# Kernel optimization log

Measured on AMD Instinct MI355X. Metric: run time of the kernel, lower is better.

## Reference

```python
import jax, jax.numpy as jnp
import numpy as np

N, E, F, H, C, K = 50000, 1600000, 128, 64, 40, 4


def setup_inputs() -> dict:
    key = jax.random.key(0)
    ks = jax.random.split(key, 4)
    x = jax.random.normal(ks[0], (N, F), dtype=jnp.float32)
    edge_index = jax.random.randint(ks[1], (2, E), 0, N, dtype=jnp.int32)
    edge_weight = jnp.ones((E,), dtype=jnp.float32)
    # lin of ChebConv: Linear(K*in, out); kaiming for layer1, xavier-ish for layer2
    W1 = jax.random.normal(ks[2], (K * F, H), dtype=jnp.float32) * (2.0 / (K * F)) ** 0.5
    b1 = jnp.zeros((H,), jnp.float32)
    W2 = jax.random.normal(ks[3], (K * H, C), dtype=jnp.float32) * (2.0 / (K * H + C)) ** 0.5
    b2 = jnp.zeros((C,), jnp.float32)
    return {"x": x, "edge_index": edge_index, "edge_weight": edge_weight,
            "W1": W1, "b1": b1, "W2": W2, "b2": b2}


def _cheb_norm(edge_index, edge_weight, num_nodes):
    """Edge weights of L_hat = 2*L/lambda_max - I with sym norm, lambda_max=2.
    L = I - D^{-1/2} A D^{-1/2}; so L_hat off-diag = -d_i^{-1/2} w d_j^{-1/2},
    diag = (1 if deg>0 else 0) - 1."""
    src, dst = edge_index[0], edge_index[1]
    deg = jax.ops.segment_sum(edge_weight, src, num_segments=num_nodes)
    dis = jnp.where(deg > 0, jax.lax.rsqrt(jnp.maximum(deg, 1e-12)), 0.0)
    w_norm = -dis[src] * edge_weight * dis[dst]   # [E] off-diagonal of L_hat
    diag = jnp.where(deg > 0, 0.0, -1.0)          # [N] diagonal of L_hat
    return src, dst, w_norm, diag


def _cheb_conv(x, src, dst, w_norm, diag, W, b, num_nodes):
    def prop(h):  # L_hat @ h via gather-multiply-scatter
        msg = w_norm[:, None] * h[src]                                  # [E, F]
        return diag[:, None] * h + jax.ops.segment_sum(msg, dst, num_segments=num_nodes)

    Tx_prev2 = x
    Tx_prev1 = prop(x)
    Txs = [Tx_prev2, Tx_prev1]
    for _ in range(2, K):
        Tx = 2.0 * prop(Tx_prev1) - Tx_prev2
        Txs.append(Tx)
        Tx_prev2, Tx_prev1 = Tx_prev1, Tx
    Z = jnp.concatenate(Txs, axis=1)              # [N, K*F]
    return Z @ W + b


def reference(x, edge_index, edge_weight, W1, b1, W2, b2):
    num_nodes = x.shape[0]
    src, dst, w_norm, diag = _cheb_norm(edge_index, edge_weight, num_nodes)
    # dropout layers are identity at inference
    h = _cheb_conv(x, src, dst, w_norm, diag, W1, b1, num_nodes)
    h = jax.nn.relu(h)
    out = _cheb_conv(h, src, dst, w_norm, diag, W2, b2, num_nodes)
    return out
```

## Files before the change

kernel.cpp:

```cpp
#include <hip/hip_runtime.h>

#define NN 50000
#define EE 1600000
#define FF 128
#define HH 64
#define CC 40

#define NCH 64
#define CHE (EE / NCH)
#define NSL 4
#define SLN (NN / NSL)

#define PA 250
#define EPP (EE / PA)
#define SB 250
#define SLNB 200
#define BCAP 64

static __device__ __forceinline__ float bf2f(unsigned short u) {
    union { unsigned int i; float f; } c; c.i = ((unsigned int)u) << 16; return c.f;
}
static __device__ __forceinline__ unsigned short f2bf(float x) {
    union { float f; unsigned int i; } c; c.f = x;
    unsigned int r = c.i + 0x7FFFu + ((c.i >> 16) & 1u);
    return (unsigned short)(r >> 16);
}

__global__ __launch_bounds__(1024) void deg_hist_kernel(
    const int* __restrict__ src, const float* __restrict__ w,
    float* __restrict__ pdeg) {
    __shared__ float ldeg[SLN];
    int s = blockIdx.x % NSL;
    int c = blockIdx.x / NSL;
    int base = s * SLN;
    for (int i = threadIdx.x; i < SLN; i += 1024) ldeg[i] = 0.f;
    __syncthreads();
    int e0 = c * CHE;
    for (int e = e0 + threadIdx.x; e < e0 + CHE; e += 1024) {
        int se = src[e];
        unsigned us = (unsigned)(se - base);
        if (us < SLN) atomicAdd(&ldeg[us], w[e]);
    }
    __syncthreads();
    for (int i = threadIdx.x; i < SLN; i += 1024)
        pdeg[(size_t)c * NN + base + i] = ldeg[i];
}

__global__ void reduce_kernel(const float* __restrict__ pdeg,
                              float* __restrict__ dis, float* __restrict__ diag) {
    int n = blockIdx.x * blockDim.x + threadIdx.x;
    if (n >= NN) return;
    float dsum = 0.f;
    for (int c = 0; c < NCH; ++c) dsum += pdeg[(size_t)c * NN + n];
    dis[n]  = (dsum > 0.f) ? rsqrtf(fmaxf(dsum, 1e-12f)) : 0.f;
    diag[n] = (dsum > 0.f) ? 0.f : -1.f;
}

__global__ __launch_bounds__(256) void bucketA_kernel(
    const int* __restrict__ src, const int* __restrict__ dst,
    const float* __restrict__ w, const float* __restrict__ dis,
    uint2* __restrict__ buckets, int* __restrict__ counts) {
    __shared__ int lcnt[SB];
    int p = blockIdx.x;
    for (int i = threadIdx.x; i < SB; i += 256) lcnt[i] = 0;
    __syncthreads();
    int e0 = p * EPP;
    for (int e = e0 + threadIdx.x; e < e0 + EPP; e += 256) {
        int de = dst[e], se = src[e];
        int sl = de / SLNB;
        int dl = de - sl * SLNB;
        float wn = -dis[se] * w[e] * dis[de];
        unsigned lo = (unsigned)se | ((unsigned)f2bf(wn) << 16);
        int idx = atomicAdd(&lcnt[sl], 1);
        buckets[((size_t)p * SB + sl) * BCAP + idx] = make_uint2(lo, (unsigned)dl);
    }
    __syncthreads();
    for (int i = threadIdx.x; i < SB; i += 256) counts[p * SB + i] = lcnt[i];
}

__global__ void scanS_kernel(const int* __restrict__ counts, int* __restrict__ sbase) {
    __shared__ int sh[256];
    int t = threadIdx.x;
    int total = 0;
    if (t < SB)
        for (int p = 0; p < PA; ++p) total += counts[p * SB + t];
    sh[t] = total;
    __syncthreads();
    for (int off = 1; off < 256; off <<= 1) {
        int x = (t >= off) ? sh[t - off] : 0;
        __syncthreads();
        sh[t] += x;
        __syncthreads();
    }
    if (t < SB) sbase[t] = sh[t] - total;
    if (t == SB - 1) sbase[SB] = sh[t];
}

__global__ __launch_bounds__(256) void bucketB_kernel(
    const uint2* __restrict__ buckets, const int* __restrict__ counts,
    const int* __restrict__ sbase,
    int* __restrict__ row_start, unsigned int* __restrict__ csr) {
    __shared__ int lhist[SLNB];
    __shared__ int sh[256];
    int s = blockIdx.x;
    int t = threadIdx.x;
    int lane = t & 63, wave = t >> 6;
    for (int i = t; i < SLNB; i += 256) lhist[i] = 0;
    __syncthreads();
    for (int p = wave; p < PA; p += 4) {
        int c = counts[p * SB + s];
        const uint2* b = buckets + ((size_t)p * SB + s) * BCAP;
        for (int i = lane; i < c; i += 64)
            atomicAdd(&lhist[b[i].y], 1);
    }
    __syncthreads();
    int v = (t < SLNB) ? lhist[t] : 0;
    sh[t] = v;
    __syncthreads();
    for (int off = 1; off < 256; off <<= 1) {
        int x = (t >= off) ? sh[t - off] : 0;
        __syncthreads();
        sh[t] += x;
        __syncthreads();
    }
    int base = sbase[s];
    if (t < SLNB) {
        int excl = sh[t] - v;
        row_start[s * SLNB + t] = base + excl;
        lhist[t] = base + excl;
    }
    if (s == SB - 1 && t == 0) row_start[NN] = sbase[SB];
    __syncthreads();
    for (int p = wave; p < PA; p += 4) {
        int c = counts[p * SB + s];
        const uint2* b = buckets + ((size_t)p * SB + s) * BCAP;
        for (int i = lane; i < c; i += 64) {
            uint2 en = b[i];
            int pos = atomicAdd(&lhist[en.y], 1);
            csr[pos] = en.x;
        }
    }
}

template <int FACT, typename OUT_T>
__global__ __launch_bounds__(256) void prop2_kernel(
    const unsigned short* __restrict__ a, int aStride, float alphaL,
    const float* __restrict__ p1, float beta1,
    const float* __restrict__ p2, float beta2, int pStride,
    const float* __restrict__ bias, int doRelu, int FOUT, int outStride,
    const float* __restrict__ diag, const int* __restrict__ rs,
    const unsigned int* __restrict__ csr, OUT_T* __restrict__ out) {
    int lane = threadIdx.x & 63;
    int wave = threadIdx.x >> 6;
    int n = blockIdx.x * 4 + wave;
    int f = lane;
    float acc = 0.f;
    if (f < FACT) {
        acc = diag[n] * bf2f(a[(size_t)n * aStride + f]);
        int j0 = rs[n], j1 = rs[n + 1];
        int j = j0;
        for (; j + 8 <= j1; j += 8) {
            unsigned cw[8];
            #pragma unroll
            for (int u = 0; u < 8; ++u) cw[u] = csr[j + u];
            float v[8];
            #pragma unroll
            for (int u = 0; u < 8; ++u)
                v[u] = bf2f(a[(size_t)(cw[u] & 0xFFFFu) * aStride + f]);
            #pragma unroll
            for (int u = 0; u < 8; ++u)
                acc = fmaf(bf2f((unsigned short)(cw[u] >> 16)), v[u], acc);
        }
        for (; j < j1; ++j) {
            unsigned cw = csr[j];
            acc = fmaf(bf2f((unsigned short)(cw >> 16)),
                       bf2f(a[(size_t)(cw & 0xFFFFu) * aStride + f]), acc);
        }
    }
    if (f < FOUT) {
        float r = alphaL * acc + beta1 * p1[(size_t)n * pStride + f];
        if (beta2 != 0.f) r = fmaf(beta2, p2[(size_t)n * pStride + f], r);
        if (bias) r += bias[f];
        if (doRelu) r = fmaxf(r, 0.f);
        OUT_T o;
        if constexpr (sizeof(OUT_T) == 2) o = f2bf(r); else o = r;
        out[(size_t)n * outStride + f] = o;
    }
}

__global__ __launch_bounds__(256) void gemm1_kernel(
    const float* __restrict__ x, const float* __restrict__ W,
    float* __restrict__ Yf, unsigned short* __restrict__ y3b) {
    __shared__ float As[64][36];
    __shared__ float Bs[32][64];
    int t = threadIdx.x;
    int m0 = blockIdx.x * 64;
    int ct = blockIdx.y;
    int tr = t / 16, tc = t % 16;
    int kq = t % 8,  ms = t / 8;
    int jb = t % 16, fb = t / 16;
    float acc[4][4] = {};
    for (int kb = 0; kb < 4; ++kb) {
        __syncthreads();
        #pragma unroll
        for (int p = 0; p < 2; ++p) {
            int m = ms + 32 * p;
            int row = m0 + m;
            float4 vv = make_float4(0.f, 0.f, 0.f, 0.f);
            if (row < NN) vv = *(const float4*)(x + (size_t)row * FF + kb * 32 + kq * 4);
            *(float4*)&As[m][kq * 4] = vv;
        }
        const float* Wb = W + ((size_t)ct * 128 + kb * 32) * HH;
        #pragma unroll
        for (int p = 0; p < 2; ++p) {
            int fi = fb + 16 * p;
            float4 vv = *(const float4*)(Wb + fi * HH + jb * 4);
            *(float4*)&Bs[fi][jb * 4] = vv;
        }
        __syncthreads();
        #pragma unroll 8
        for (int k = 0; k < 32; ++k) {
            float a0 = As[tr * 4 + 0][k], a1 = As[tr * 4 + 1][k];
            float a2 = As[tr * 4 + 2][k], a3 = As[tr * 4 + 3][k];
            float4 b = *(float4*)&Bs[k][tc * 4];
            acc[0][0] = fmaf(a0, b.x, acc[0][0]); acc[0][1] = fmaf(a0, b.y, acc[0][1]);
            acc[0][2] = fmaf(a0, b.z, acc[0][2]); acc[0][3] = fmaf(a0, b.w, acc[0][3]);
            acc[1][0] = fmaf(a1, b.x, acc[1][0]); acc[1][1] = fmaf(a1, b.y, acc[1][1]);
            acc[1][2] = fmaf(a1, b.z, acc[1][2]); acc[1][3] = fmaf(a1, b.w, acc[1][3]);
            acc[2][0] = fmaf(a2, b.x, acc[2][0]); acc[2][1] = fmaf(a2, b.y, acc[2][1]);
            acc[2][2] = fmaf(a2, b.z, acc[2][2]); acc[2][3] = fmaf(a2, b.w, acc[2][3]);
            acc[3][0] = fmaf(a3, b.x, acc[3][0]); acc[3][1] = fmaf(a3, b.y, acc[3][1]);
            acc[3][2] = fmaf(a3, b.z, acc[3][2]); acc[3][3] = fmaf(a3, b.w, acc[3][3]);
        }
    }
    #pragma unroll
    for (int r = 0; r < 4; ++r) {
        int n = m0 + tr * 4 + r;
        if (n < NN) {
            *(float4*)(Yf + (size_t)n * 256 + ct * 64 + tc * 4) =
                make_float4(acc[r][0], acc[r][1], acc[r][2], acc[r][3]);
            if (ct == 3) {
                ushort4 u4;
                u4.x = f2bf(acc[r][0]); u4.y = f2bf(acc[r][1]);
                u4.z = f2bf(acc[r][2]); u4.w = f2bf(acc[r][3]);
                *(ushort4*)(y3b + (size_t)n * 64 + tc * 4) = u4;
            }
        }
    }
}

__global__ __launch_bounds__(256) void gemm2_kernel(
    const float* __restrict__ h, const float* __restrict__ W,
    float* __restrict__ Y2f, unsigned short* __restrict__ y3b2) {
    __shared__ float As[128][36];
    __shared__ float Bs[32][40];
    int t = threadIdx.x;
    int m0 = blockIdx.x * 128;
    int kt = blockIdx.y;
    int tr = t / 8, tc = t % 8;
    int kq = t % 8, ms = t / 8;
    float acc[4][5] = {};
    for (int kb = 0; kb < 2; ++kb) {
        __syncthreads();
        #pragma unroll
        for (int p = 0; p < 4; ++p) {
            int m = ms + 32 * p;
            int row = m0 + m;
            float4 vv = make_float4(0.f, 0.f, 0.f, 0.f);
            if (row < NN) vv = *(const float4*)(h + (size_t)row * HH + kb * 32 + kq * 4);
            *(float4*)&As[m][kq * 4] = vv;
        }
        const float* Wb = W + ((size_t)kt * 64 + kb * 32) * CC;
        for (int i = t; i < 32 * CC; i += 256) ((float*)Bs)[i] = Wb[i];
        __syncthreads();
        #pragma unroll 4
        for (int k = 0; k < 32; ++k) {
            float a0 = As[tr * 4 + 0][k], a1 = As[tr * 4 + 1][k];
            float a2 = As[tr * 4 + 2][k], a3 = As[tr * 4 + 3][k];
            #pragma unroll
            for (int c = 0; c < 5; ++c) {
                float b = Bs[k][tc * 5 + c];
                acc[0][c] = fmaf(a0, b, acc[0][c]);
                acc[1][c] = fmaf(a1, b, acc[1][c]);
                acc[2][c] = fmaf(a2, b, acc[2][c]);
                acc[3][c] = fmaf(a3, b, acc[3][c]);
            }
        }
    }
    #pragma unroll
    for (int r = 0; r < 4; ++r) {
        int n = m0 + tr * 4 + r;
        if (n < NN) {
            float* orow = Y2f + (size_t)n * 256 + kt * 64;
            #pragma unroll
            for (int c = 0; c < 5; ++c) orow[tc * 5 + c] = acc[r][c];
            if (tc < 6) {
                #pragma unroll
                for (int c = 0; c < 4; ++c) orow[40 + tc * 4 + c] = 0.f;
            }
            if (kt == 3) {
                unsigned short* brow = y3b2 + (size_t)n * 64;
                #pragma unroll
                for (int c = 0; c < 5; ++c) brow[tc * 5 + c] = f2bf(acc[r][c]);
                if (tc < 6) {
                    #pragma unroll
                    for (int c = 0; c < 4; ++c) brow[40 + tc * 4 + c] = 0;
                }
            }
        }
    }
}

extern "C" void kernel_launch(void* const* d_in, const int* in_sizes, int n_in,
                              void* d_out, int out_size, void* d_ws, size_t ws_size,
                              hipStream_t stream) {
    const float* x    = (const float*)d_in[0];
    const int*   eidx = (const int*)d_in[1];
    const float* ew   = (const float*)d_in[2];
    const float* W1   = (const float*)d_in[3];
    const float* b1   = (const float*)d_in[4];
    const float* W2   = (const float*)d_in[5];
    const float* b2   = (const float*)d_in[6];
    float* out = (float*)d_out;

    const int* src = eidx;
    const int* dst = eidx + EE;

    float* p = (float*)d_ws;
    unsigned int* csr = (unsigned int*)p;  p += (size_t)EE;
    float* dis  = p;                  p += ((NN + 63) / 64) * 64;
    float* diag = p;                  p += ((NN + 63) / 64) * 64;
    float* Yf   = p;                  p += (size_t)NN * 256;
    unsigned short* y3b = (unsigned short*)p;  p += (size_t)NN * 32;
    unsigned short* u   = (unsigned short*)p;  p += (size_t)NN * 32;
    unsigned short* v   = (unsigned short*)p;  p += (size_t)NN * 32;
    float* h    = p;                  p += (size_t)NN * 64;
    int* row_start = (int*)p;
    int* counts    = row_start + NN + 1;
    int* sbase     = counts + PA * SB;

    float* pdeg    = Yf;
    uint2* buckets = (uint2*)(Yf + (size_t)64 * NN);
    float* Y2f = Yf;
    unsigned short* y3b2 = y3b;
    unsigned short* u2 = u;
    unsigned short* v2 = v;

    const int B = 256;
    deg_hist_kernel<<<NCH * NSL, 1024, 0, stream>>>(src, ew, pdeg);
    reduce_kernel<<<(NN + B - 1) / B, B, 0, stream>>>(pdeg, dis, diag);
    bucketA_kernel<<<PA, 256, 0, stream>>>(src, dst, ew, dis, buckets, counts);
    scanS_kernel<<<1, 256, 0, stream>>>(counts, sbase);
    bucketB_kernel<<<SB, 256, 0, stream>>>(buckets, counts, sbase, row_start, csr);

    int pgrid = NN / 4;

    gemm1_kernel<<<dim3((NN + 63) / 64, 4), 256, 0, stream>>>(x, W1, Yf, y3b);
    prop2_kernel<64, unsigned short><<<pgrid, 256, 0, stream>>>(
        y3b, 64, 4.f, Yf + 128, 2.f, nullptr, 0.f, 256,
        nullptr, 0, 64, 64, diag, row_start, csr, u);
    prop2_kernel<64, unsigned short><<<pgrid, 256, 0, stream>>>(
        u, 64, 1.f, Yf + 64, 1.f, Yf + 192, -3.f, 256,
        nullptr, 0, 64, 64, diag, row_start, csr, v);
    prop2_kernel<64, float><<<pgrid, 256, 0, stream>>>(
        v, 64, 1.f, Yf, 1.f, Yf + 128, -1.f, 256,
        b1, 1, 64, 64, diag, row_start, csr, h);

    gemm2_kernel<<<dim3((NN + 127) / 128, 4), 256, 0, stream>>>(h, W2, Y2f, y3b2);
    prop2_kernel<48, unsigned short><<<pgrid, 256, 0, stream>>>(
        y3b2, 64, 4.f, Y2f + 128, 2.f, nullptr, 0.f, 256,
        nullptr, 0, 48, 64, diag, row_start, csr, u2);
    prop2_kernel<48, unsigned short><<<pgrid, 256, 0, stream>>>(
        u2, 64, 1.f, Y2f + 64, 1.f, Y2f + 192, -3.f, 256,
        nullptr, 0, 48, 64, diag, row_start, csr, v2);
    prop2_kernel<48, float><<<pgrid, 256, 0, stream>>>(
        v2, 64, 1.f, Y2f, 1.f, Y2f + 128, -1.f, 256,
        b2, 0, 40, 40, diag, row_start, csr, out);
}
```

Measured before the change: 575.5 us.

## Split layer-1 propagation into two 32-feature halves with dual-edge lanes

Layer-1 bf16 intermediate features are stored as two separate 32-column arrays. Each propagation step now runs as two launches, one per half, so the gather working set per pass is halved and is more likely to stay in cache. Within a wave, the two 32-lane halves process alternate edges with unrolled independent loads and nontemporal hints, then combine partial sums with a shuffle. The bucketing kernel also caches counts in shared memory and uses 16-lane groups per partition. The cost is twice as many CSR reads and kernel launches for layer 1.

```diff
diff --git a/kernel.cpp b/kernel.cpp
--- a/kernel.cpp
+++ b/kernel.cpp
@@ -100,17 +100,19 @@
     const uint2* __restrict__ buckets, const int* __restrict__ counts,
     const int* __restrict__ sbase,
     int* __restrict__ row_start, unsigned int* __restrict__ csr) {
+    __shared__ int lcounts[PA];
     __shared__ int lhist[SLNB];
     __shared__ int sh[256];
     int s = blockIdx.x;
     int t = threadIdx.x;
-    int lane = t & 63, wave = t >> 6;
+    if (t < PA) lcounts[t] = counts[t * SB + s];
     for (int i = t; i < SLNB; i += 256) lhist[i] = 0;
     __syncthreads();
-    for (int p = wave; p < PA; p += 4) {
-        int c = counts[p * SB + s];
+    int g = t >> 4, l16 = t & 15;
+    for (int p = g; p < PA; p += 16) {
+        int c = lcounts[p];
         const uint2* b = buckets + ((size_t)p * SB + s) * BCAP;
-        for (int i = lane; i < c; i += 64)
+        for (int i = l16; i < c; i += 16)
             atomicAdd(&lhist[b[i].y], 1);
     }
     __syncthreads();
@@ -131,14 +133,70 @@
     }
     if (s == SB - 1 && t == 0) row_start[NN] = sbase[SB];
     __syncthreads();
-    for (int p = wave; p < PA; p += 4) {
-        int c = counts[p * SB + s];
+    for (int p = g; p < PA; p += 16) {
+        int c = lcounts[p];
         const uint2* b = buckets + ((size_t)p * SB + s) * BCAP;
-        for (int i = lane; i < c; i += 64) {
+        for (int i = l16; i < c; i += 16) {
             uint2 en = b[i];
             int pos = atomicAdd(&lhist[en.y], 1);
             csr[pos] = en.x;
         }
+    }
+}
+
+template <typename OUT_T>
+__global__ __launch_bounds__(256) void prop_half_kernel(
+    const unsigned short* __restrict__ a,
+    float alphaL,
+    const float* __restrict__ p1, float beta1,
+    const float* __restrict__ p2, float beta2,
+    const float* __restrict__ bias, int doRelu, int outStride,
+    const float* __restrict__ diag, const int* __restrict__ rs,
+    const unsigned int* __restrict__ csr, OUT_T* __restrict__ out) {
+    int lane = threadIdx.x & 63;
+    int wave = threadIdx.x >> 6;
+    int n = blockIdx.x * 4 + wave;
+    int f = lane & 31;
+    int es = lane >> 5;
+    float acc = 0.f;
+    int j0 = rs[n], j1 = rs[n + 1];
+    int j = j0;
+    for (; j + 16 <= j1; j += 16) {
+        unsigned cw[8];
+        #pragma unroll
+        for (int u = 0; u < 8; ++u)
+            cw[u] = __builtin_nontemporal_load(csr + j + 2 * u + es);
+        float v[8];
+        #pragma unroll
+        for (int u = 0; u < 8; ++u)
+            v[u] = bf2f(a[(size_t)(cw[u] & 0xFFFFu) * 32 + f]);
+        #pragma unroll
+        for (int u = 0; u < 8; ++u)
+            acc = fmaf(bf2f((unsigned short)(cw[u] >> 16)), v[u], acc);
+    }
+    for (; j + 2 <= j1; j += 2) {
+        unsigned cw = __builtin_nontemporal_load(csr + j + es);
+        acc = fmaf(bf2f((unsigned short)(cw >> 16)),
+                   bf2f(a[(size_t)(cw & 0xFFFFu) * 32 + f]), acc);
+    }
+    if (j < j1 && es == 0) {
+        unsigned cw = __builtin_nontemporal_load(csr + j);
+        acc = fmaf(bf2f((unsigned short)(cw >> 16)),
+                   bf2f(a[(size_t)(cw & 0xFFFFu) * 32 + f]), acc);
+    }
+    acc += __shfl_down(acc, 32);
+    if (es == 0) {
+        acc = fmaf(diag[n], bf2f(a[(size_t)n * 32 + f]), acc);
+        float r = alphaL * acc
+                + beta1 * __builtin_nontemporal_load(p1 + (size_t)n * 256 + f);
+        if (beta2 != 0.f)
+            r = fmaf(beta2, __builtin_nontemporal_load(p2 + (size_t)n * 256 + f), r);
+        if (bias) r += bias[f];
+        if (doRelu) r = fmaxf(r, 0.f);
+        if constexpr (sizeof(OUT_T) == 2)
+            __builtin_nontemporal_store(f2bf(r), out + (size_t)n * outStride + f);
+        else
+            __builtin_nontemporal_store(r, out + (size_t)n * outStride + f);
     }
 }
 
@@ -190,7 +248,8 @@
 
 __global__ __launch_bounds__(256) void gemm1_kernel(
     const float* __restrict__ x, const float* __restrict__ W,
-    float* __restrict__ Yf, unsigned short* __restrict__ y3b) {
+    float* __restrict__ Yf, unsigned short* __restrict__ y3lo,
+    unsigned short* __restrict__ y3hi) {
     __shared__ float As[64][36];
     __shared__ float Bs[32][64];
     int t = threadIdx.x;
@@ -243,7 +302,10 @@
                 ushort4 u4;
                 u4.x = f2bf(acc[r][0]); u4.y = f2bf(acc[r][1]);
                 u4.z = f2bf(acc[r][2]); u4.w = f2bf(acc[r][3]);
-                *(ushort4*)(y3b + (size_t)n * 64 + tc * 4) = u4;
+                int j = tc * 4;
+                unsigned short* dstp = (j < 32) ? (y3lo + (size_t)n * 32 + j)
+                                                : (y3hi + (size_t)n * 32 + (j - 32));
+                *(ushort4*)dstp = u4;
             }
         }
     }
@@ -331,20 +393,27 @@
     float* dis  = p;                  p += ((NN + 63) / 64) * 64;
     float* diag = p;                  p += ((NN + 63) / 64) * 64;
     float* Yf   = p;                  p += (size_t)NN * 256;
-    unsigned short* y3b = (unsigned short*)p;  p += (size_t)NN * 32;
-    unsigned short* u   = (unsigned short*)p;  p += (size_t)NN * 32;
-    unsigned short* v   = (unsigned short*)p;  p += (size_t)NN * 32;
+    unsigned short* hv1 = (unsigned short*)p;  p += (size_t)NN * 32;
+    unsigned short* hv2 = (unsigned short*)p;  p += (size_t)NN * 32;
+    unsigned short* hv3 = (unsigned short*)p;  p += (size_t)NN * 32;
     float* h    = p;                  p += (size_t)NN * 64;
     int* row_start = (int*)p;
     int* counts    = row_start + NN + 1;
     int* sbase     = counts + PA * SB;
 
+    unsigned short* y3lo = hv1;
+    unsigned short* y3hi = hv1 + (size_t)NN * 32;
+    unsigned short* ulo  = hv2;
+    unsigned short* uhi  = hv2 + (size_t)NN * 32;
+    unsigned short* vlo  = hv3;
+    unsigned short* vhi  = hv3 + (size_t)NN * 32;
+
     float* pdeg    = Yf;
     uint2* buckets = (uint2*)(Yf + (size_t)64 * NN);
     float* Y2f = Yf;
-    unsigned short* y3b2 = y3b;
-    unsigned short* u2 = u;
-    unsigned short* v2 = v;
+    unsigned short* y3b2 = hv1;
+    unsigned short* u2 = hv2;
+    unsigned short* v2 = hv3;
 
     const int B = 256;
     deg_hist_kernel<<<NCH * NSL, 1024, 0, stream>>>(src, ew, pdeg);
@@ -355,16 +424,25 @@
 
     int pgrid = NN / 4;
 
-    gemm1_kernel<<<dim3((NN + 63) / 64, 4), 256, 0, stream>>>(x, W1, Yf, y3b);
-    prop2_kernel<64, unsigned short><<<pgrid, 256, 0, stream>>>(
-        y3b, 64, 4.f, Yf + 128, 2.f, nullptr, 0.f, 256,
-        nullptr, 0, 64, 64, diag, row_start, csr, u);
-    prop2_kernel<64, unsigned short><<<pgrid, 256, 0, stream>>>(
-        u, 64, 1.f, Yf + 64, 1.f, Yf + 192, -3.f, 256,
-        nullptr, 0, 64, 64, diag, row_start, csr, v);
-    prop2_kernel<64, float><<<pgrid, 256, 0, stream>>>(
-        v, 64, 1.f, Yf, 1.f, Yf + 128, -1.f, 256,
-        b1, 1, 64, 64, diag, row_start, csr, h);
+    gemm1_kernel<<<dim3((NN + 63) / 64, 4), 256, 0, stream>>>(x, W1, Yf, y3lo, y3hi);
+    prop_half_kernel<unsigned short><<<pgrid, 256, 0, stream>>>(
+        y3lo, 4.f, Yf + 128 + 0, 2.f, nullptr, 0.f, nullptr, 0, 32,
+        diag, row_start, csr, ulo);
+    prop_half_kernel<unsigned short><<<pgrid, 256, 0, stream>>>(
+        y3hi, 4.f, Yf + 128 + 32, 2.f, nullptr, 0.f, nullptr, 0, 32,
+        diag, row_start, csr, uhi);
+    prop_half_kernel<unsigned short><<<pgrid, 256, 0, stream>>>(
+        ulo, 1.f, Yf + 64 + 0, 1.f, Yf + 192 + 0, -3.f, nullptr, 0, 32,
+        diag, row_start, csr, vlo);
+    prop_half_kernel<unsigned short><<<pgrid, 256, 0, stream>>>(
+        uhi, 1.f, Yf + 64 + 32, 1.f, Yf + 192 + 32, -3.f, nullptr, 0, 32,
+        diag, row_start, csr, vhi);
+    prop_half_kernel<float><<<pgrid, 256, 0, stream>>>(
+        vlo, 1.f, Yf + 0 + 0, 1.f, Yf + 128 + 0, -1.f, b1 + 0, 1, 64,
+        diag, row_start, csr, h);
+    prop_half_kernel<float><<<pgrid, 256, 0, stream>>>(
+        vhi, 1.f, Yf + 0 + 32, 1.f, Yf + 128 + 32, -1.f, b1 + 32, 1, 64,
+        diag, row_start, csr, h + 32);
 
     gemm2_kernel<<<dim3((NN + 127) / 128, 4), 256, 0, stream>>>(h, W2, Y2f, y3b2);
     prop2_kernel<48, unsigned short><<<pgrid, 256, 0, stream>>>(
```

After: 675.4 us. 17.4% more time.

## Store GEMM Chebyshev slabs in bf16 and widen bucketB counts parallelism

Applied to the files above, without the earlier changes.

The GEMM outputs Y=X·W_k for all four Chebyshev terms are now stored as separate bf16 slabs instead of an fp32 [N,256] buffer. The prop kernels read the p1/p2 combination terms in bf16 at a fixed stride. This cuts write and read bytes for the linear terms but adds bf16 rounding to terms that were fp32 before. Separately, bucketB caches per-partition counts in shared memory and uses 16-lane groups instead of wavefronts, since bucket sizes are small. Bucket scratch moves to a dedicated workspace region.

```diff
diff --git a/kernel.cpp b/kernel.cpp
--- a/kernel.cpp
+++ b/kernel.cpp
@@ -100,17 +100,19 @@
     const uint2* __restrict__ buckets, const int* __restrict__ counts,
     const int* __restrict__ sbase,
     int* __restrict__ row_start, unsigned int* __restrict__ csr) {
+    __shared__ int lcounts[PA];
     __shared__ int lhist[SLNB];
     __shared__ int sh[256];
     int s = blockIdx.x;
     int t = threadIdx.x;
-    int lane = t & 63, wave = t >> 6;
+    if (t < PA) lcounts[t] = counts[t * SB + s];
     for (int i = t; i < SLNB; i += 256) lhist[i] = 0;
     __syncthreads();
-    for (int p = wave; p < PA; p += 4) {
-        int c = counts[p * SB + s];
+    int g = t >> 4, l16 = t & 15;
+    for (int p = g; p < PA; p += 16) {
+        int c = lcounts[p];
         const uint2* b = buckets + ((size_t)p * SB + s) * BCAP;
-        for (int i = lane; i < c; i += 64)
+        for (int i = l16; i < c; i += 16)
             atomicAdd(&lhist[b[i].y], 1);
     }
     __syncthreads();
@@ -131,10 +133,10 @@
     }
     if (s == SB - 1 && t == 0) row_start[NN] = sbase[SB];
     __syncthreads();
-    for (int p = wave; p < PA; p += 4) {
-        int c = counts[p * SB + s];
+    for (int p = g; p < PA; p += 16) {
+        int c = lcounts[p];
         const uint2* b = buckets + ((size_t)p * SB + s) * BCAP;
-        for (int i = lane; i < c; i += 64) {
+        for (int i = l16; i < c; i += 16) {
             uint2 en = b[i];
             int pos = atomicAdd(&lhist[en.y], 1);
             csr[pos] = en.x;
@@ -144,9 +146,9 @@
 
 template <int FACT, typename OUT_T>
 __global__ __launch_bounds__(256) void prop2_kernel(
-    const unsigned short* __restrict__ a, int aStride, float alphaL,
-    const float* __restrict__ p1, float beta1,
-    const float* __restrict__ p2, float beta2, int pStride,
+    const unsigned short* __restrict__ a, float alphaL,
+    const unsigned short* __restrict__ p1, float beta1,
+    const unsigned short* __restrict__ p2, float beta2,
     const float* __restrict__ bias, int doRelu, int FOUT, int outStride,
     const float* __restrict__ diag, const int* __restrict__ rs,
     const unsigned int* __restrict__ csr, OUT_T* __restrict__ out) {
@@ -156,7 +158,7 @@
     int f = lane;
     float acc = 0.f;
     if (f < FACT) {
-        acc = diag[n] * bf2f(a[(size_t)n * aStride + f]);
+        acc = diag[n] * bf2f(a[(size_t)n * 64 + f]);
         int j0 = rs[n], j1 = rs[n + 1];
         int j = j0;
         for (; j + 8 <= j1; j += 8) {
@@ -166,7 +168,7 @@
             float v[8];
             #pragma unroll
             for (int u = 0; u < 8; ++u)
-                v[u] = bf2f(a[(size_t)(cw[u] & 0xFFFFu) * aStride + f]);
+                v[u] = bf2f(a[(size_t)(cw[u] & 0xFFFFu) * 64 + f]);
             #pragma unroll
             for (int u = 0; u < 8; ++u)
                 acc = fmaf(bf2f((unsigned short)(cw[u] >> 16)), v[u], acc);
@@ -174,12 +176,12 @@
         for (; j < j1; ++j) {
             unsigned cw = csr[j];
             acc = fmaf(bf2f((unsigned short)(cw >> 16)),
-                       bf2f(a[(size_t)(cw & 0xFFFFu) * aStride + f]), acc);
+                       bf2f(a[(size_t)(cw & 0xFFFFu) * 64 + f]), acc);
         }
     }
     if (f < FOUT) {
-        float r = alphaL * acc + beta1 * p1[(size_t)n * pStride + f];
-        if (beta2 != 0.f) r = fmaf(beta2, p2[(size_t)n * pStride + f], r);
+        float r = alphaL * acc + beta1 * bf2f(p1[(size_t)n * 64 + f]);
+        if (beta2 != 0.f) r = fmaf(beta2, bf2f(p2[(size_t)n * 64 + f]), r);
         if (bias) r += bias[f];
         if (doRelu) r = fmaxf(r, 0.f);
         OUT_T o;
@@ -190,7 +192,7 @@
 
 __global__ __launch_bounds__(256) void gemm1_kernel(
     const float* __restrict__ x, const float* __restrict__ W,
-    float* __restrict__ Yf, unsigned short* __restrict__ y3b) {
+    unsigned short* __restrict__ Yb) {
     __shared__ float As[64][36];
     __shared__ float Bs[32][64];
     int t = threadIdx.x;
@@ -233,25 +235,22 @@
             acc[3][2] = fmaf(a3, b.z, acc[3][2]); acc[3][3] = fmaf(a3, b.w, acc[3][3]);
         }
     }
+    unsigned short* slab = Yb + (size_t)ct * NN * 64;
     #pragma unroll
     for (int r = 0; r < 4; ++r) {
         int n = m0 + tr * 4 + r;
         if (n < NN) {
-            *(float4*)(Yf + (size_t)n * 256 + ct * 64 + tc * 4) =
-                make_float4(acc[r][0], acc[r][1], acc[r][2], acc[r][3]);
-            if (ct == 3) {
-                ushort4 u4;
-                u4.x = f2bf(acc[r][0]); u4.y = f2bf(acc[r][1]);
-                u4.z = f2bf(acc[r][2]); u4.w = f2bf(acc[r][3]);
-                *(ushort4*)(y3b + (size_t)n * 64 + tc * 4) = u4;
-            }
+            ushort4 u4;
+            u4.x = f2bf(acc[r][0]); u4.y = f2bf(acc[r][1]);
+            u4.z = f2bf(acc[r][2]); u4.w = f2bf(acc[r][3]);
+            *(ushort4*)(slab + (size_t)n * 64 + tc * 4) = u4;
         }
     }
 }
 
 __global__ __launch_bounds__(256) void gemm2_kernel(
     const float* __restrict__ h, const float* __restrict__ W,
-    float* __restrict__ Y2f, unsigned short* __restrict__ y3b2) {
+    unsigned short* __restrict__ Zb) {
     __shared__ float As[128][36];
     __shared__ float Bs[32][40];
     int t = threadIdx.x;
@@ -287,25 +286,17 @@
             }
         }
     }
+    unsigned short* slab = Zb + (size_t)kt * NN * 64;
     #pragma unroll
     for (int r = 0; r < 4; ++r) {
         int n = m0 + tr * 4 + r;
         if (n < NN) {
-            float* orow = Y2f + (size_t)n * 256 + kt * 64;
-            #pragma unroll
-            for (int c = 0; c < 5; ++c) orow[tc * 5 + c] = acc[r][c];
+            unsigned short* brow = slab + (size_t)n * 64;
+            #pragma unroll
+            for (int c = 0; c < 5; ++c) brow[tc * 5 + c] = f2bf(acc[r][c]);
             if (tc < 6) {
                 #pragma unroll
-                for (int c = 0; c < 4; ++c) orow[40 + tc * 4 + c] = 0.f;
-            }
-            if (kt == 3) {
-                unsigned short* brow = y3b2 + (size_t)n * 64;
-                #pragma unroll
-                for (int c = 0; c < 5; ++c) brow[tc * 5 + c] = f2bf(acc[r][c]);
-                if (tc < 6) {
-                    #pragma unroll
-                    for (int c = 0; c < 4; ++c) brow[40 + tc * 4 + c] = 0;
-                }
+                for (int c = 0; c < 4; ++c) brow[40 + tc * 4 + c] = 0;
             }
         }
     }
@@ -330,19 +321,26 @@
     unsigned int* csr = (unsigned int*)p;  p += (size_t)EE;
     float* dis  = p;                  p += ((NN + 63) / 64) * 64;
     float* diag = p;                  p += ((NN + 63) / 64) * 64;
-    float* Yf   = p;                  p += (size_t)NN * 256;
-    unsigned short* y3b = (unsigned short*)p;  p += (size_t)NN * 32;
-    unsigned short* u   = (unsigned short*)p;  p += (size_t)NN * 32;
-    unsigned short* v   = (unsigned short*)p;  p += (size_t)NN * 32;
+    unsigned short* Yb = (unsigned short*)p;  p += (size_t)NN * 128;
+    unsigned short* u  = (unsigned short*)p;  p += (size_t)NN * 32;
+    unsigned short* v  = (unsigned short*)p;  p += (size_t)NN * 32;
     float* h    = p;                  p += (size_t)NN * 64;
+    float* scratch = p;               p += (size_t)PA * SB * BCAP * 2;
     int* row_start = (int*)p;
     int* counts    = row_start + NN + 1;
     int* sbase     = counts + PA * SB;
 
-    float* pdeg    = Yf;
-    uint2* buckets = (uint2*)(Yf + (size_t)64 * NN);
-    float* Y2f = Yf;
-    unsigned short* y3b2 = y3b;
+    float* pdeg    = scratch;
+    uint2* buckets = (uint2*)scratch;
+    unsigned short* y0b = Yb;
+    unsigned short* y1b = Yb + (size_t)1 * NN * 64;
+    unsigned short* y2b = Yb + (size_t)2 * NN * 64;
+    unsigned short* y3b = Yb + (size_t)3 * NN * 64;
+    unsigned short* Zb = Yb;
+    unsigned short* z0 = Zb;
+    unsigned short* z1 = Zb + (size_t)1 * NN * 64;
+    unsigned short* z2 = Zb + (size_t)2 * NN * 64;
+    unsigned short* z3 = Zb + (size_t)3 * NN * 64;
     unsigned short* u2 = u;
     unsigned short* v2 = v;
 
@@ -355,25 +353,25 @@
 
     int pgrid = NN / 4;
 
-    gemm1_kernel<<<dim3((NN + 63) / 64, 4), 256, 0, stream>>>(x, W1, Yf, y3b);
+    gemm1_kernel<<<dim3((NN + 63) / 64, 4), 256, 0, stream>>>(x, W1, Yb);
     prop2_kernel<64, unsigned short><<<pgrid, 256, 0, stream>>>(
-        y3b, 64, 4.f, Yf + 128, 2.f, nullptr, 0.f, 256,
+        y3b, 4.f, y2b, 2.f, nullptr, 0.f,
         nullptr, 0, 64, 64, diag, row_start, csr, u);
     prop2_kernel<64, unsigned short><<<pgrid, 256, 0, stream>>>(
-        u, 64, 1.f, Yf + 64, 1.f, Yf + 192, -3.f, 256,
+        u, 1.f, y1b, 1.f, y3b, -3.f,
         nullptr, 0, 64, 64, diag, row_start, csr, v);
     prop2_kernel<64, float><<<pgrid, 256, 0, stream>>>(
-        v, 64, 1.f, Yf, 1.f, Yf + 128, -1.f, 256,
+        v, 1.f, y0b, 1.f, y2b, -1.f,
         b1, 1, 64, 64, diag, row_start, csr, h);
 
-    gemm2_kernel<<<dim3((NN + 127) / 128, 4), 256, 0, stream>>>(h, W2, Y2f, y3b2);
+    gemm2_kernel<<<dim3((NN + 127) / 128, 4), 256, 0, stream>>>(h, W2, Zb);
     prop2_kernel<48, unsigned short><<<pgrid, 256, 0, stream>>>(
-        y3b2, 64, 4.f, Y2f + 128, 2.f, nullptr, 0.f, 256,
+        z3, 4.f, z2, 2.f, nullptr, 0.f,
         nullptr, 0, 48, 64, diag, row_start, csr, u2);
     prop2_kernel<48, unsigned short><<<pgrid, 256, 0, stream>>>(
-        u2, 64, 1.f, Y2f + 64, 1.f, Y2f + 192, -3.f, 256,
+        u2, 1.f, z1, 1.f, z3, -3.f,
         nullptr, 0, 48, 64, diag, row_start, csr, v2);
     prop2_kernel<48, float><<<pgrid, 256, 0, stream>>>(
-        v2, 64, 1.f, Y2f, 1.f, Y2f + 128, -1.f, 256,
+        v2, 1.f, z0, 1.f, z2, -1.f,
         b2, 0, 40, 40, diag, row_start, csr, out);
 }
```

New measurement: 525.5 us. 8.7% less time.
